# Kernel tuning notes

Hardware: AMD Instinct MI355X
Metric: run time of the kernel (lower is better)

The kernel has to match this reference:

```python
import jax, jax.numpy as jnp
import numpy as np

D_MODEL = 256
NHEAD = 8
HEAD_DIM = D_MODEL // NHEAD
EPS_ATTN = 1e-6
EPS_LN = 1e-5


def layer_norm(x, g, b):
    mu = jnp.mean(x, axis=-1, keepdims=True)
    var = jnp.mean(jnp.square(x - mu), axis=-1, keepdims=True)
    return (x - mu) * jax.lax.rsqrt(var + EPS_LN) * g + b


def setup_inputs() -> dict:
    key = jax.random.key(0)
    ks = jax.random.split(key, 9)
    N, L, S = 8, 8192, 8192
    d = D_MODEL
    sc = 1.0 / np.sqrt(d)
    return {
        "x": jax.random.normal(ks[0], (N, L, d), dtype=jnp.float32),
        "source": jax.random.normal(ks[1], (N, S, d), dtype=jnp.float32),
        "Wq": jax.random.normal(ks[2], (d, d), dtype=jnp.float32) * sc,
        "Wk": jax.random.normal(ks[3], (d, d), dtype=jnp.float32) * sc,
        "Wv": jax.random.normal(ks[4], (d, d), dtype=jnp.float32) * sc,
        "Wm": jax.random.normal(ks[5], (d, d), dtype=jnp.float32) * sc,
        "W1": jax.random.normal(ks[6], (2 * d, d), dtype=jnp.float32) * (1.0 / np.sqrt(2 * d)),
        "W2": jax.random.normal(ks[7], (d, d), dtype=jnp.float32) * sc,
        "g1": jnp.ones((d,), jnp.float32),
        "b1": jnp.zeros((d,), jnp.float32),
        "g2": jnp.ones((d,), jnp.float32),
        "b2": jnp.zeros((d,), jnp.float32),
    }


def linear_attention(q, k, v):
    # q: [N,L,H,D], k,v: [N,S,H,D]
    Q = jax.nn.elu(q) + 1.0
    K = jax.nn.elu(k) + 1.0
    S = v.shape[1]
    v = v / S
    KV = jnp.einsum('nshd,nshv->nhdv', K, v)          # [N,H,D,D]
    Z = 1.0 / (jnp.einsum('nlhd,nhd->nlh', Q, K.sum(axis=1)) + EPS_ATTN)
    out = jnp.einsum('nlhd,nhdv,nlh->nlhv', Q, KV, Z) * S
    return out


def reference(x, source, Wq, Wk, Wv, Wm, W1, W2, g1, b1, g2, b2):
    N, L, _ = x.shape
    q = (x @ Wq).reshape(N, L, NHEAD, HEAD_DIM)
    k = (source @ Wk).reshape(N, -1, NHEAD, HEAD_DIM)
    v = (source @ Wv).reshape(N, -1, NHEAD, HEAD_DIM)
    msg = linear_attention(q, k, v).reshape(N, L, D_MODEL)
    msg = layer_norm(msg @ Wm, g1, b1)
    msg = jnp.concatenate([x, msg], axis=2)
    msg = jax.nn.relu(msg @ W1) @ W2
    msg = layer_norm(msg, g2, b2)
    return x + msg
```

## Files before the change

### kernel.cpp

```cpp
#include <hip/hip_runtime.h>

typedef __attribute__((ext_vector_type(4))) float f32x4;
typedef __attribute__((ext_vector_type(8))) short short8;
typedef __attribute__((ext_vector_type(4))) unsigned short us4;
typedef __attribute__((ext_vector_type(8))) unsigned short us8;

#define D_MODEL 256
#define SEQ 8192L
#define NBATCH 8
#define TOTROWS 65536L

__device__ inline unsigned short f2bf(float f){
  unsigned int u = __float_as_uint(f);
  u += 0x7fffu + ((u >> 16) & 1u);
  return (unsigned short)(u >> 16);
}
__device__ inline float bf2f(unsigned short h){
  return __uint_as_float(((unsigned int)h) << 16);
}
__device__ inline f32x4 mfma16(short8 a, short8 b, f32x4 c){
  return __builtin_amdgcn_mfma_f32_16x16x32_bf16(a, b, c, 0, 0, 0);
}
__device__ inline us8 pack8(f32x4 a, f32x4 b){
  us8 o;
  o[0]=f2bf(a[0]); o[1]=f2bf(a[1]); o[2]=f2bf(a[2]); o[3]=f2bf(a[3]);
  o[4]=f2bf(b[0]); o[5]=f2bf(b[1]); o[6]=f2bf(b[2]); o[7]=f2bf(b[3]);
  return o;
}
__device__ inline void gl16(const unsigned short* g, unsigned short* lds){
  __builtin_amdgcn_global_load_lds(
      (const __attribute__((address_space(1))) unsigned int*)g,
      (__attribute__((address_space(3))) unsigned int*)lds, 16, 0, 0);
}

__global__ __launch_bounds__(256) void conv_f32_to_bf16(
    const float* __restrict__ s, unsigned short* __restrict__ d){
  const long N = TOTROWS * 256 / 8;
  for(long c = (long)blockIdx.x * 256 + threadIdx.x; c < N;
      c += (long)gridDim.x * 256){
    long off = c * 8;
    f32x4 v0 = *(const f32x4*)(s + off);
    f32x4 v1 = *(const f32x4*)(s + off + 4);
    *(us8*)(d + off) = pack8(v0, v1);
  }
}

__global__ void prep_weights(const float* __restrict__ Wq, const float* __restrict__ Wk,
                             const float* __restrict__ Wv, const float* __restrict__ Wm,
                             const float* __restrict__ W1, const float* __restrict__ W2,
                             unsigned short* __restrict__ WT){
  int o = blockIdx.x * 256 + threadIdx.x;
  int m = o >> 16, rem = o & 65535, n = rem >> 8, k = rem & 255;
  const float* s;
  switch(m){
    case 0: s = Wq; break;
    case 1: s = Wk; break;
    case 2: s = Wv; break;
    case 3: s = Wm; break;
    case 4: s = W1; break;
    case 5: s = W1 + 65536; break;
    default: s = W2; break;
  }
  WT[o] = f2bf(s[k * 256 + n]);
}

__global__ __launch_bounds__(256) void kv_proj(
    const unsigned short* __restrict__ srcb, const unsigned short* __restrict__ WT,
    unsigned short* __restrict__ Kw, unsigned short* __restrict__ Vw)
{
  __shared__ unsigned short As[2][128][32];
  __shared__ unsigned short Bs[2][128][32];
  const int t = threadIdx.x, lane = t & 63, wid = t >> 6;
  const int l16 = lane & 15, g4 = lane >> 4;
  const int wr = (wid >> 1) * 64, wc = (wid & 1) * 64;
  const int mb = blockIdx.x, nb = blockIdx.y;
  const long rowbase = (long)mb * 128;
  const unsigned short* Wsl = WT + (nb < 2 ? 1 : 2) * 65536 + (nb & 1) * 128 * 256;
  const int sr = lane >> 2, sc = (lane & 3) * 8;

  auto STAGE = [&](int buf, int kb){
    #pragma unroll
    for(int j = 0; j < 2; j++){
      int r0 = wid * 32 + j * 16;
      gl16(srcb + (rowbase + r0 + sr) * 256 + kb + sc, &As[buf][r0][0]);
      gl16(Wsl  + (long)(r0 + sr) * 256 + kb + sc,     &Bs[buf][r0][0]);
    }
  };

  f32x4 acc[4][4] = {};
  STAGE(0, 0);
  __syncthreads();
  int cur = 0;
  for(int it = 0; it < 8; it++){
    if(it < 7) STAGE(cur ^ 1, (it + 1) * 32);
    short8 afr[4], bfr[4];
    #pragma unroll
    for(int mi = 0; mi < 4; mi++) afr[mi] = *(const short8*)&As[cur][wr + mi*16 + l16][g4*8];
    #pragma unroll
    for(int ni = 0; ni < 4; ni++) bfr[ni] = *(const short8*)&Bs[cur][wc + ni*16 + l16][g4*8];
    #pragma unroll
    for(int mi = 0; mi < 4; mi++)
      #pragma unroll
      for(int ni = 0; ni < 4; ni++)
        acc[mi][ni] = mfma16(afr[mi], bfr[ni], acc[mi][ni]);
    __syncthreads();
    cur ^= 1;
  }

  const bool isK = nb < 2;
  unsigned short* dst = isK ? Kw : Vw;
  const int colbase = (nb & 1) * 128 + wc;
  #pragma unroll
  for(int mi = 0; mi < 4; mi++)
    #pragma unroll
    for(int ni = 0; ni < 4; ni++)
      #pragma unroll
      for(int rr = 0; rr < 4; rr++){
        long row = rowbase + wr + mi*16 + g4*4 + rr;
        int col = colbase + ni*16 + l16;
        float v = acc[mi][ni][rr];
        v = isK ? (v > 0.f ? v + 1.f : __expf(v)) : v * (1.f / 8192.f);
        dst[row * 256 + col] = f2bf(v);
      }
}

__global__ __launch_bounds__(256) void kv_acc(const unsigned short* __restrict__ Kw,
                                              const unsigned short* __restrict__ Vw,
                                              float* __restrict__ part){
  const int c = blockIdx.x;
  const int n = blockIdx.y;
  const int t = threadIdx.x;
  const int h = t >> 5, d = t & 31;
  const long base = ((long)n * SEQ + (long)c * 128) * 256;
  float acc[32];
  #pragma unroll
  for(int j = 0; j < 32; j++) acc[j] = 0.f;
  float ks = 0.f;
  for(int rr = 0; rr < 128; rr++){
    const unsigned short* Kr = Kw + base + (long)rr * 256;
    const unsigned short* Vr = Vw + base + (long)rr * 256;
    float kv = bf2f(Kr[h * 32 + d]);
    ks += kv;
    #pragma unroll
    for(int q = 0; q < 4; q++){
      us8 vv = *(const us8*)(Vr + h * 32 + q * 8);
      #pragma unroll
      for(int j = 0; j < 8; j++) acc[q*8 + j] += kv * bf2f(vv[j]);
    }
  }
  float* p = part + ((long)(n * 64 + c) * 33) * 256;
  #pragma unroll
  for(int v = 0; v < 32; v++) p[v * 256 + t] = acc[v];
  p[32 * 256 + t] = ks;
}

__global__ void kv_red(const float* __restrict__ part, float* __restrict__ KVws){
  const int v = blockIdx.x;
  const int n = blockIdx.y;
  const int t = threadIdx.x;
  float s = 0.f;
  for(int c = 0; c < 64; c++) s += part[((long)(n * 64 + c) * 33 + v) * 256 + t];
  KVws[((long)n * 33 + v) * 256 + t] = s;
}

__global__ __launch_bounds__(256) void attn_kern(
    const unsigned short* __restrict__ xb, const unsigned short* __restrict__ WT,
    const float* __restrict__ KVws, const float* __restrict__ g1,
    const float* __restrict__ b1, unsigned short* __restrict__ msgln)
{
  __shared__ unsigned short As[2][64][32];
  __shared__ unsigned short Bu[2][256][32];
  __shared__ float zs[64][8];
  __shared__ float ksl[256];
  __shared__ unsigned short R[64][264];

  const int t = threadIdx.x, lane = t & 63, wid = t >> 6;
  const int l16 = lane & 15, g4 = lane >> 4;
  const int wc = wid * 64;
  const int mb = blockIdx.x;
  const long rowbase = (long)mb * 64;
  const int n = mb >> 7;
  const int sr = lane >> 2, sc = (lane & 3) * 8;

  const unsigned short* wq = WT;
  const unsigned short* wm = WT + 3 * 65536;

  auto STAGE1 = [&](int buf, int kb){
    gl16(xb + (rowbase + wid*16 + sr) * 256 + kb + sc, &As[buf][wid*16][0]);
    #pragma unroll
    for(int j = 0; j < 4; j++){
      int r0 = wid * 64 + j * 16;
      gl16(wq + (long)(r0 + sr) * 256 + kb + sc, &Bu[buf][r0][0]);
    }
  };
  auto STAGE6 = [&](int buf, int kb){
    #pragma unroll
    for(int j = 0; j < 4; j++){
      int r0 = wid * 64 + j * 16;
      gl16(wm + (long)(r0 + sr) * 256 + kb + sc, &Bu[buf][r0][0]);
    }
  };

  f32x4 acc[4][4] = {};
  STAGE1(0, 0);
  __syncthreads();
  int cur = 0;
  for(int it = 0; it < 8; it++){
    if(it < 7) STAGE1(cur ^ 1, (it + 1) * 32);
    short8 afr[4], bfr[4];
    #pragma unroll
    for(int mi = 0; mi < 4; mi++) afr[mi] = *(const short8*)&As[cur][mi*16 + l16][g4*8];
    #pragma unroll
    for(int ni = 0; ni < 4; ni++) bfr[ni] = *(const short8*)&Bu[cur][wc + ni*16 + l16][g4*8];
    #pragma unroll
    for(int mi = 0; mi < 4; mi++)
      #pragma unroll
      for(int ni = 0; ni < 4; ni++)
        acc[mi][ni] = mfma16(afr[mi], bfr[ni], acc[mi][ni]);
    __syncthreads();
    cur ^= 1;
  }

  #pragma unroll
  for(int mi = 0; mi < 4; mi++)
    #pragma unroll
    for(int ni = 0; ni < 4; ni++)
      #pragma unroll
      for(int rr = 0; rr < 4; rr++){
        float v = acc[mi][ni][rr];
        v = v > 0.f ? v + 1.f : __expf(v);
        R[mi*16 + g4*4 + rr][wc + ni*16 + l16] = f2bf(v);
      }

  {
    const float* kvn = KVws + (long)n * 33 * 256;
    const int vv = t & 31, hh = t >> 5;
    #pragma unroll
    for(int d = 0; d < 32; d += 4){
      f32x4 w = *(const f32x4*)(kvn + vv * 256 + hh * 32 + d);
      us4 o; o[0]=f2bf(w[0]); o[1]=f2bf(w[1]); o[2]=f2bf(w[2]); o[3]=f2bf(w[3]);
      *(us4*)&Bu[0][t][d] = o;
    }
    ksl[t] = kvn[32 * 256 + t];
  }
  __syncthreads();

  #pragma unroll
  for(int pp = 0; pp < 2; pp++){
    int p = t + pp * 256;
    int row = p >> 3, h = p & 7;
    float s = 0.f;
    #pragma unroll
    for(int d = 0; d < 32; d++) s += bf2f(R[row][h*32 + d]) * ksl[h*32 + d];
    zs[row][h] = 1.f / (s + 1e-6f);
  }
  __syncthreads();

  f32x4 acc2[4][4];
  #pragma unroll
  for(int ni = 0; ni < 4; ni++){
    const int cb = wc + ni * 16;
    const int h = cb >> 5;
    short8 b = *(const short8*)&Bu[0][cb + l16][g4*8];
    #pragma unroll
    for(int mi = 0; mi < 4; mi++){
      short8 a = *(const short8*)&R[mi*16 + l16][h*32 + g4*8];
      f32x4 zz = {0.f, 0.f, 0.f, 0.f};
      acc2[mi][ni] = mfma16(a, b, zz);
    }
  }
  STAGE6(1, 0);
  #pragma unroll
  for(int mi = 0; mi < 4; mi++)
    #pragma unroll
    for(int ni = 0; ni < 4; ni++){
      const int h = (wc + ni * 16) >> 5;
      #pragma unroll
      for(int rr = 0; rr < 4; rr++){
        int row = mi*16 + g4*4 + rr;
        acc2[mi][ni][rr] *= zs[row][h] * 8192.f;
      }
    }
  __syncthreads();
  #pragma unroll
  for(int mi = 0; mi < 4; mi++)
    #pragma unroll
    for(int ni = 0; ni < 4; ni++)
      #pragma unroll
      for(int rr = 0; rr < 4; rr++)
        R[mi*16 + g4*4 + rr][wc + ni*16 + l16] = f2bf(acc2[mi][ni][rr]);
  __syncthreads();

  f32x4 acc3[4][4] = {};
  cur = 1;
  for(int it = 0; it < 8; it++){
    if(it < 7) STAGE6(cur ^ 1, (it + 1) * 32);
    int kb = it * 32;
    short8 afr[4], bfr[4];
    #pragma unroll
    for(int mi = 0; mi < 4; mi++) afr[mi] = *(const short8*)&R[mi*16 + l16][kb + g4*8];
    #pragma unroll
    for(int ni = 0; ni < 4; ni++) bfr[ni] = *(const short8*)&Bu[cur][wc + ni*16 + l16][g4*8];
    #pragma unroll
    for(int mi = 0; mi < 4; mi++)
      #pragma unroll
      for(int ni = 0; ni < 4; ni++)
        acc3[mi][ni] = mfma16(afr[mi], bfr[ni], acc3[mi][ni]);
    __syncthreads();
    cur ^= 1;
  }

  #pragma unroll
  for(int mi = 0; mi < 4; mi++)
    #pragma unroll
    for(int ni = 0; ni < 4; ni++)
      #pragma unroll
      for(int rr = 0; rr < 4; rr++)
        R[mi*16 + g4*4 + rr][wc + ni*16 + l16] = f2bf(acc3[mi][ni][rr]);
  __syncthreads();

  {
    int row = t >> 2, q = t & 3;
    float s = 0.f, ss = 0.f;
    #pragma unroll
    for(int j8 = 0; j8 < 8; j8++){
      us8 vv = *(const us8*)&R[row][q*64 + j8*8];
      #pragma unroll
      for(int e = 0; e < 8; e++){ float v = bf2f(vv[e]); s += v; ss += v * v; }
    }
    s  += __shfl_xor(s, 1);  ss += __shfl_xor(ss, 1);
    s  += __shfl_xor(s, 2);  ss += __shfl_xor(ss, 2);
    float mu  = s * (1.f / 256.f);
    float var = ss * (1.f / 256.f) - mu * mu;
    float rs  = rsqrtf(var + 1e-5f);
    unsigned short* orow = msgln + (rowbase + row) * 256 + q * 64;
    const float* g1p = g1 + q * 64;
    const float* b1p = b1 + q * 64;
    #pragma unroll
    for(int j8 = 0; j8 < 8; j8++){
      us8 vv = *(const us8*)&R[row][q*64 + j8*8];
      us8 o;
      #pragma unroll
      for(int e = 0; e < 8; e++){
        float v = (bf2f(vv[e]) - mu) * rs * g1p[j8*8 + e] + b1p[j8*8 + e];
        o[e] = f2bf(v);
      }
      *(us8*)(orow + j8*8) = o;
    }
  }
}

__global__ __launch_bounds__(256) void ffn_kern(
    const float* __restrict__ x, const unsigned short* __restrict__ xb,
    const unsigned short* __restrict__ WT,
    const unsigned short* __restrict__ msgln, const float* __restrict__ g2,
    const float* __restrict__ b2, float* __restrict__ out)
{
  __shared__ unsigned short As[2][64][32];
  __shared__ unsigned short Bs[2][256][32];
  __shared__ unsigned short R[64][264];
  const int t = threadIdx.x, lane = t & 63, wid = t >> 6;
  const int l16 = lane & 15, g4 = lane >> 4;
  const int wc = wid * 64;
  const long rowbase = (long)blockIdx.x * 64;
  const int sr = lane >> 2, sc = (lane & 3) * 8;

  auto STAGE1 = [&](int buf, int it){
    int kb = (it & 7) * 32;
    const unsigned short* asrc = (it < 8) ? xb : msgln;
    gl16(asrc + (rowbase + wid*16 + sr) * 256 + kb + sc, &As[buf][wid*16][0]);
    const unsigned short* wsl = WT + (it < 8 ? 4 : 5) * 65536;
    #pragma unroll
    for(int j = 0; j < 4; j++){
      int r0 = wid * 64 + j * 16;
      gl16(wsl + (long)(r0 + sr) * 256 + kb + sc, &Bs[buf][r0][0]);
    }
  };
  const unsigned short* w2 = WT + 6 * 65536;
  auto STAGE2 = [&](int buf, int kb){
    #pragma unroll
    for(int j = 0; j < 4; j++){
      int r0 = wid * 64 + j * 16;
      gl16(w2 + (long)(r0 + sr) * 256 + kb + sc, &Bs[buf][r0][0]);
    }
  };

  f32x4 acc[4][4] = {};
  STAGE1(0, 0);
  __syncthreads();
  int cur = 0;
  for(int it = 0; it < 16; it++){
    if(it < 15) STAGE1(cur ^ 1, it + 1);
    short8 afr[4], bfr[4];
    #pragma unroll
    for(int mi = 0; mi < 4; mi++) afr[mi] = *(const short8*)&As[cur][mi*16 + l16][g4*8];
    #pragma unroll
    for(int ni = 0; ni < 4; ni++) bfr[ni] = *(const short8*)&Bs[cur][wc + ni*16 + l16][g4*8];
    #pragma unroll
    for(int mi = 0; mi < 4; mi++)
      #pragma unroll
      for(int ni = 0; ni < 4; ni++)
        acc[mi][ni] = mfma16(afr[mi], bfr[ni], acc[mi][ni]);
    __syncthreads();
    cur ^= 1;
  }
  STAGE2(0, 0);

  #pragma unroll
  for(int mi = 0; mi < 4; mi++)
    #pragma unroll
    for(int ni = 0; ni < 4; ni++)
      #pragma unroll
      for(int rr = 0; rr < 4; rr++){
        float v = acc[mi][ni][rr];
        R[mi*16 + g4*4 + rr][wc + ni*16 + l16] = f2bf(v > 0.f ? v : 0.f);
      }
  __syncthreads();

  f32x4 acc2[4][4] = {};
  cur = 0;
  for(int it = 0; it < 8; it++){
    if(it < 7) STAGE2(cur ^ 1, (it + 1) * 32);
    int kb = it * 32;
    short8 afr[4], bfr[4];
    #pragma unroll
    for(int mi = 0; mi < 4; mi++) afr[mi] = *(const short8*)&R[mi*16 + l16][kb + g4*8];
    #pragma unroll
    for(int ni = 0; ni < 4; ni++) bfr[ni] = *(const short8*)&Bs[cur][wc + ni*16 + l16][g4*8];
    #pragma unroll
    for(int mi = 0; mi < 4; mi++)
      #pragma unroll
      for(int ni = 0; ni < 4; ni++)
        acc2[mi][ni] = mfma16(afr[mi], bfr[ni], acc2[mi][ni]);
    __syncthreads();
    cur ^= 1;
  }

  #pragma unroll
  for(int mi = 0; mi < 4; mi++)
    #pragma unroll
    for(int ni = 0; ni < 4; ni++)
      #pragma unroll
      for(int rr = 0; rr < 4; rr++)
        R[mi*16 + g4*4 + rr][wc + ni*16 + l16] = f2bf(acc2[mi][ni][rr]);
  __syncthreads();

  {
    int row = t >> 2, q = t & 3;
    float s = 0.f, ss = 0.f;
    #pragma unroll
    for(int j8 = 0; j8 < 8; j8++){
      us8 vv = *(const us8*)&R[row][q*64 + j8*8];
      #pragma unroll
      for(int e = 0; e < 8; e++){ float v = bf2f(vv[e]); s += v; ss += v * v; }
    }
    s  += __shfl_xor(s, 1);  ss += __shfl_xor(ss, 1);
    s  += __shfl_xor(s, 2);  ss += __shfl_xor(ss, 2);
    float mu  = s * (1.f / 256.f);
    float var = ss * (1.f / 256.f) - mu * mu;
    float rs  = rsqrtf(var + 1e-5f);
    const float* xr = x + (rowbase + row) * 256 + q * 64;
    float* orow = out + (rowbase + row) * 256 + q * 64;
    const float* g2p = g2 + q * 64;
    const float* b2p = b2 + q * 64;
    #pragma unroll
    for(int j4 = 0; j4 < 16; j4++){
      f32x4 xv = *(const f32x4*)(xr + j4 * 4);
      f32x4 o;
      #pragma unroll
      for(int e = 0; e < 4; e++){
        int idx = j4 * 4 + e;
        float v = (bf2f(R[row][q*64 + idx]) - mu) * rs * g2p[idx] + b2p[idx];
        o[e] = xv[e] + v;
      }
      *(f32x4*)(orow + j4 * 4) = o;
    }
  }
}

extern "C" void kernel_launch(void* const* d_in, const int* in_sizes, int n_in,
                              void* d_out, int out_size, void* d_ws, size_t ws_size,
                              hipStream_t stream)
{
  const float* x   = (const float*)d_in[0];
  const float* src = (const float*)d_in[1];
  const float* Wq  = (const float*)d_in[2];
  const float* Wk  = (const float*)d_in[3];
  const float* Wv  = (const float*)d_in[4];
  const float* Wm  = (const float*)d_in[5];
  const float* W1  = (const float*)d_in[6];
  const float* W2  = (const float*)d_in[7];
  const float* g1  = (const float*)d_in[8];
  const float* b1  = (const float*)d_in[9];
  const float* g2  = (const float*)d_in[10];
  const float* b2  = (const float*)d_in[11];

  char* ws = (char*)d_ws;
  unsigned short* WT   = (unsigned short*)(ws);
  unsigned short* srcb = (unsigned short*)(ws + (1ul  << 20));
  float*          part = (float*)         (ws + (1ul  << 20));
  unsigned short* xb   = (unsigned short*)(ws + (1ul  << 20));
  unsigned short* Kw   = (unsigned short*)(ws + (33ul << 20));
  unsigned short* msgl = Kw;
  unsigned short* Vw   = (unsigned short*)(ws + (65ul << 20));
  float*          KVws = (float*)         (ws + (97ul << 20));

  prep_weights<<<1792, 256, 0, stream>>>(Wq, Wk, Wv, Wm, W1, W2, WT);
  conv_f32_to_bf16<<<2048, 256, 0, stream>>>(src, srcb);
  kv_proj<<<dim3(512, 4), 256, 0, stream>>>(srcb, WT, Kw, Vw);
  kv_acc<<<dim3(64, 8), 256, 0, stream>>>(Kw, Vw, part);
  kv_red<<<dim3(33, 8), 256, 0, stream>>>(part, KVws);
  conv_f32_to_bf16<<<2048, 256, 0, stream>>>(x, xb);
  attn_kern<<<1024, 256, 0, stream>>>(xb, WT, KVws, g1, b1, msgl);
  ffn_kern<<<1024, 256, 0, stream>>>(x, xb, WT, msgl, g2, b2, (float*)d_out);
}
```

Measured before the change: 419.9 us.

## Fuse attention and FFN kernels, convert x to bf16 inline

Merges attn_kern and ffn_kern into one kernel, so the layer-normed message stays in shared memory and is never written to or read back from global memory. The separate x float-to-bf16 conversion kernel is also removed. x is now read as fp32 and packed to bf16 inside the GEMM staging, which is a synchronous register path instead of the async gl16 copy. This saves two kernel launches and the global round trips for xb and msgln, but the x tile is loaded twice and the longer fused kernel may use more registers.

```diff
diff --git a/kernel.cpp b/kernel.cpp
--- a/kernel.cpp
+++ b/kernel.cpp
@@ -163,13 +163,14 @@
   KVws[((long)n * 33 + v) * 256 + t] = s;
 }
 
-__global__ __launch_bounds__(256) void attn_kern(
-    const unsigned short* __restrict__ xb, const unsigned short* __restrict__ WT,
+__global__ __launch_bounds__(256) void attnffn(
+    const float* __restrict__ x, const unsigned short* __restrict__ WT,
     const float* __restrict__ KVws, const float* __restrict__ g1,
-    const float* __restrict__ b1, unsigned short* __restrict__ msgln)
+    const float* __restrict__ b1, const float* __restrict__ g2,
+    const float* __restrict__ b2, float* __restrict__ out)
 {
   __shared__ unsigned short As[2][64][32];
-  __shared__ unsigned short Bu[2][256][32];
+  __shared__ unsigned short Bs[2][256][32];
   __shared__ float zs[64][8];
   __shared__ float ksl[256];
   __shared__ unsigned short R[64][264];
@@ -184,34 +185,34 @@
 
   const unsigned short* wq = WT;
   const unsigned short* wm = WT + 3 * 65536;
-
-  auto STAGE1 = [&](int buf, int kb){
-    gl16(xb + (rowbase + wid*16 + sr) * 256 + kb + sc, &As[buf][wid*16][0]);
+  const unsigned short* w2 = WT + 6 * 65536;
+
+  auto STAGE_X = [&](int buf, int kb){
+    int row = wid * 16 + sr;
+    const float* g = x + (rowbase + row) * 256 + kb + sc;
+    f32x4 v0 = *(const f32x4*)g;
+    f32x4 v1 = *(const f32x4*)(g + 4);
+    *(us8*)&As[buf][row][sc] = pack8(v0, v1);
+  };
+  auto STAGE_B = [&](const unsigned short* w, int buf, int kb){
     #pragma unroll
     for(int j = 0; j < 4; j++){
       int r0 = wid * 64 + j * 16;
-      gl16(wq + (long)(r0 + sr) * 256 + kb + sc, &Bu[buf][r0][0]);
+      gl16(w + (long)(r0 + sr) * 256 + kb + sc, &Bs[buf][r0][0]);
     }
   };
-  auto STAGE6 = [&](int buf, int kb){
-    #pragma unroll
-    for(int j = 0; j < 4; j++){
-      int r0 = wid * 64 + j * 16;
-      gl16(wm + (long)(r0 + sr) * 256 + kb + sc, &Bu[buf][r0][0]);
-    }
-  };
 
   f32x4 acc[4][4] = {};
-  STAGE1(0, 0);
+  STAGE_X(0, 0); STAGE_B(wq, 0, 0);
   __syncthreads();
   int cur = 0;
   for(int it = 0; it < 8; it++){
-    if(it < 7) STAGE1(cur ^ 1, (it + 1) * 32);
+    if(it < 7){ STAGE_X(cur ^ 1, (it + 1) * 32); STAGE_B(wq, cur ^ 1, (it + 1) * 32); }
     short8 afr[4], bfr[4];
     #pragma unroll
     for(int mi = 0; mi < 4; mi++) afr[mi] = *(const short8*)&As[cur][mi*16 + l16][g4*8];
     #pragma unroll
-    for(int ni = 0; ni < 4; ni++) bfr[ni] = *(const short8*)&Bu[cur][wc + ni*16 + l16][g4*8];
+    for(int ni = 0; ni < 4; ni++) bfr[ni] = *(const short8*)&Bs[cur][wc + ni*16 + l16][g4*8];
     #pragma unroll
     for(int mi = 0; mi < 4; mi++)
       #pragma unroll
@@ -239,7 +240,7 @@
     for(int d = 0; d < 32; d += 4){
       f32x4 w = *(const f32x4*)(kvn + vv * 256 + hh * 32 + d);
       us4 o; o[0]=f2bf(w[0]); o[1]=f2bf(w[1]); o[2]=f2bf(w[2]); o[3]=f2bf(w[3]);
-      *(us4*)&Bu[0][t][d] = o;
+      *(us4*)&Bs[0][t][d] = o;
     }
     ksl[t] = kvn[32 * 256 + t];
   }
@@ -261,7 +262,7 @@
   for(int ni = 0; ni < 4; ni++){
     const int cb = wc + ni * 16;
     const int h = cb >> 5;
-    short8 b = *(const short8*)&Bu[0][cb + l16][g4*8];
+    short8 b = *(const short8*)&Bs[0][cb + l16][g4*8];
     #pragma unroll
     for(int mi = 0; mi < 4; mi++){
       short8 a = *(const short8*)&R[mi*16 + l16][h*32 + g4*8];
@@ -269,7 +270,7 @@
       acc2[mi][ni] = mfma16(a, b, zz);
     }
   }
-  STAGE6(1, 0);
+  STAGE_B(wm, 1, 0);
   #pragma unroll
   for(int mi = 0; mi < 4; mi++)
     #pragma unroll
@@ -294,13 +295,13 @@
   f32x4 acc3[4][4] = {};
   cur = 1;
   for(int it = 0; it < 8; it++){
-    if(it < 7) STAGE6(cur ^ 1, (it + 1) * 32);
+    if(it < 7) STAGE_B(wm, cur ^ 1, (it + 1) * 32);
     int kb = it * 32;
     short8 afr[4], bfr[4];
     #pragma unroll
     for(int mi = 0; mi < 4; mi++) afr[mi] = *(const short8*)&R[mi*16 + l16][kb + g4*8];
     #pragma unroll
-    for(int ni = 0; ni < 4; ni++) bfr[ni] = *(const short8*)&Bu[cur][wc + ni*16 + l16][g4*8];
+    for(int ni = 0; ni < 4; ni++) bfr[ni] = *(const short8*)&Bs[cur][wc + ni*16 + l16][g4*8];
     #pragma unroll
     for(int mi = 0; mi < 4; mi++)
       #pragma unroll
@@ -319,6 +320,7 @@
         R[mi*16 + g4*4 + rr][wc + ni*16 + l16] = f2bf(acc3[mi][ni][rr]);
   __syncthreads();
 
+  STAGE_X(0, 0); STAGE_B(WT + 4 * 65536, 0, 0);
   {
     int row = t >> 2, q = t & 3;
     float s = 0.f, ss = 0.f;
@@ -333,7 +335,6 @@
     float mu  = s * (1.f / 256.f);
     float var = ss * (1.f / 256.f) - mu * mu;
     float rs  = rsqrtf(var + 1e-5f);
-    unsigned short* orow = msgln + (rowbase + row) * 256 + q * 64;
     const float* g1p = g1 + q * 64;
     const float* b1p = b1 + q * 64;
     #pragma unroll
@@ -345,66 +346,39 @@
         float v = (bf2f(vv[e]) - mu) * rs * g1p[j8*8 + e] + b1p[j8*8 + e];
         o[e] = f2bf(v);
       }
-      *(us8*)(orow + j8*8) = o;
-    }
-  }
-}
-
-__global__ __launch_bounds__(256) void ffn_kern(
-    const float* __restrict__ x, const unsigned short* __restrict__ xb,
-    const unsigned short* __restrict__ WT,
-    const unsigned short* __restrict__ msgln, const float* __restrict__ g2,
-    const float* __restrict__ b2, float* __restrict__ out)
-{
-  __shared__ unsigned short As[2][64][32];
-  __shared__ unsigned short Bs[2][256][32];
-  __shared__ unsigned short R[64][264];
-  const int t = threadIdx.x, lane = t & 63, wid = t >> 6;
-  const int l16 = lane & 15, g4 = lane >> 4;
-  const int wc = wid * 64;
-  const long rowbase = (long)blockIdx.x * 64;
-  const int sr = lane >> 2, sc = (lane & 3) * 8;
-
-  auto STAGE1 = [&](int buf, int it){
-    int kb = (it & 7) * 32;
-    const unsigned short* asrc = (it < 8) ? xb : msgln;
-    gl16(asrc + (rowbase + wid*16 + sr) * 256 + kb + sc, &As[buf][wid*16][0]);
-    const unsigned short* wsl = WT + (it < 8 ? 4 : 5) * 65536;
-    #pragma unroll
-    for(int j = 0; j < 4; j++){
-      int r0 = wid * 64 + j * 16;
-      gl16(wsl + (long)(r0 + sr) * 256 + kb + sc, &Bs[buf][r0][0]);
-    }
-  };
-  const unsigned short* w2 = WT + 6 * 65536;
-  auto STAGE2 = [&](int buf, int kb){
-    #pragma unroll
-    for(int j = 0; j < 4; j++){
-      int r0 = wid * 64 + j * 16;
-      gl16(w2 + (long)(r0 + sr) * 256 + kb + sc, &Bs[buf][r0][0]);
-    }
-  };
-
-  f32x4 acc[4][4] = {};
-  STAGE1(0, 0);
-  __syncthreads();
-  int cur = 0;
+      *(us8*)&R[row][q*64 + j8*8] = o;
+    }
+  }
+  __syncthreads();
+
+  f32x4 acch[4][4] = {};
+  cur = 0;
   for(int it = 0; it < 16; it++){
-    if(it < 15) STAGE1(cur ^ 1, it + 1);
+    if(it < 15){
+      int nit = it + 1, kb = (nit & 7) * 32;
+      if(nit < 8) STAGE_X(cur ^ 1, kb);
+      STAGE_B(WT + (nit < 8 ? 4 : 5) * 65536, cur ^ 1, kb);
+    }
     short8 afr[4], bfr[4];
-    #pragma unroll
-    for(int mi = 0; mi < 4; mi++) afr[mi] = *(const short8*)&As[cur][mi*16 + l16][g4*8];
+    if(it < 8){
+      #pragma unroll
+      for(int mi = 0; mi < 4; mi++) afr[mi] = *(const short8*)&As[cur][mi*16 + l16][g4*8];
+    } else {
+      int kb = (it & 7) * 32;
+      #pragma unroll
+      for(int mi = 0; mi < 4; mi++) afr[mi] = *(const short8*)&R[mi*16 + l16][kb + g4*8];
+    }
     #pragma unroll
     for(int ni = 0; ni < 4; ni++) bfr[ni] = *(const short8*)&Bs[cur][wc + ni*16 + l16][g4*8];
     #pragma unroll
     for(int mi = 0; mi < 4; mi++)
       #pragma unroll
       for(int ni = 0; ni < 4; ni++)
-        acc[mi][ni] = mfma16(afr[mi], bfr[ni], acc[mi][ni]);
+        acch[mi][ni] = mfma16(afr[mi], bfr[ni], acch[mi][ni]);
     __syncthreads();
     cur ^= 1;
   }
-  STAGE2(0, 0);
+  STAGE_B(w2, 0, 0);
 
   #pragma unroll
   for(int mi = 0; mi < 4; mi++)
@@ -412,15 +386,15 @@
     for(int ni = 0; ni < 4; ni++)
       #pragma unroll
       for(int rr = 0; rr < 4; rr++){
-        float v = acc[mi][ni][rr];
+        float v = acch[mi][ni][rr];
         R[mi*16 + g4*4 + rr][wc + ni*16 + l16] = f2bf(v > 0.f ? v : 0.f);
       }
   __syncthreads();
 
-  f32x4 acc2[4][4] = {};
+  f32x4 accy[4][4] = {};
   cur = 0;
   for(int it = 0; it < 8; it++){
-    if(it < 7) STAGE2(cur ^ 1, (it + 1) * 32);
+    if(it < 7) STAGE_B(w2, cur ^ 1, (it + 1) * 32);
     int kb = it * 32;
     short8 afr[4], bfr[4];
     #pragma unroll
@@ -431,7 +405,7 @@
     for(int mi = 0; mi < 4; mi++)
       #pragma unroll
       for(int ni = 0; ni < 4; ni++)
-        acc2[mi][ni] = mfma16(afr[mi], bfr[ni], acc2[mi][ni]);
+        accy[mi][ni] = mfma16(afr[mi], bfr[ni], accy[mi][ni]);
     __syncthreads();
     cur ^= 1;
   }
@@ -442,7 +416,7 @@
     for(int ni = 0; ni < 4; ni++)
       #pragma unroll
       for(int rr = 0; rr < 4; rr++)
-        R[mi*16 + g4*4 + rr][wc + ni*16 + l16] = f2bf(acc2[mi][ni][rr]);
+        R[mi*16 + g4*4 + rr][wc + ni*16 + l16] = f2bf(accy[mi][ni][rr]);
   __syncthreads();
 
   {
@@ -499,9 +473,7 @@
   unsigned short* WT   = (unsigned short*)(ws);
   unsigned short* srcb = (unsigned short*)(ws + (1ul  << 20));
   float*          part = (float*)         (ws + (1ul  << 20));
-  unsigned short* xb   = (unsigned short*)(ws + (1ul  << 20));
   unsigned short* Kw   = (unsigned short*)(ws + (33ul << 20));
-  unsigned short* msgl = Kw;
   unsigned short* Vw   = (unsigned short*)(ws + (65ul << 20));
   float*          KVws = (float*)         (ws + (97ul << 20));
 
@@ -510,7 +482,5 @@
   kv_proj<<<dim3(512, 4), 256, 0, stream>>>(srcb, WT, Kw, Vw);
   kv_acc<<<dim3(64, 8), 256, 0, stream>>>(Kw, Vw, part);
   kv_red<<<dim3(33, 8), 256, 0, stream>>>(part, KVws);
-  conv_f32_to_bf16<<<2048, 256, 0, stream>>>(x, xb);
-  attn_kern<<<1024, 256, 0, stream>>>(xb, WT, KVws, g1, b1, msgl);
-  ffn_kern<<<1024, 256, 0, stream>>>(x, xb, WT, msgl, g2, b2, (float*)d_out);
-}
+  attnffn<<<1024, 256, 0, stream>>>(x, WT, KVws, g1, b1, g2, b2, (float*)d_out);
+}
```

Result: slower. 459.0 us (+9.3%).
